# Optimization experiments

Measured on AMD Instinct MI355X. Metric: run time of the kernel, lower is better.

Reference implementation:

```python
import jax, jax.numpy as jnp
import numpy as np

NUM_HEAD = 8


def setup_inputs() -> dict:
    key = jax.random.key(0)
    k1, k2, k3, k4 = jax.random.split(key, 4)
    B, C, H, W = 16, 512, 64, 64
    x = jax.random.normal(k1, (B, C, H, W), dtype=jnp.float32)
    w_qkv = jax.random.normal(k2, (3 * C, C), dtype=jnp.float32) * 0.02  # Conv2d 1x1, no bias
    w_proj = jax.random.normal(k3, (C, C), dtype=jnp.float32) * 0.02
    b_proj = jax.random.normal(k4, (C,), dtype=jnp.float32) * 0.02
    return {"x": x, "w_qkv": w_qkv, "w_proj": w_proj, "b_proj": b_proj}


def reference(x, w_qkv, w_proj, b_proj):
    B, C, H, W = x.shape
    nh = NUM_HEAD
    hd = C // nh
    scale = hd ** (-0.5)
    # 1x1 conv == channel matmul
    qkv = jnp.einsum('oc,bchw->bohw', w_qkv, x)  # [B, 3C, H, W]
    q, k, v = jnp.split(qkv, 3, axis=1)
    q = q.reshape(B, nh, hd, H * W)
    k = k.reshape(B, nh, hd, H * W)
    v = v.reshape(B, nh, hd, H * W)
    # NOTE: faithful to source: contracts over the spatial (last) axis,
    # producing a [B, nh, hd, hd] matrix.
    attn = jnp.einsum('bnqd,bnkd->bnqk', q, k) * scale
    attn = jax.nn.softmax(attn, axis=-1)
    # Faithful to source: 'k' and 'v' are both summed independently (outer sum),
    # exactly as torch.einsum computes it.
    out = jnp.einsum('bnqk,bnvd->bnqd', attn, v)
    out = out.reshape(B, C, H, W)
    return jnp.einsum('oc,bchw->bohw', w_proj, out) + b_proj[None, :, None, None]
```

## Files before the change

### kernel.cpp

```cpp
#include <hip/hip_runtime.h>

#define CDIM 512
#define NH 8
#define HWDIM 4096
#define BATCH 16

__global__ __launch_bounds__(256) void prep_kernel(
    const float* __restrict__ wqkv, const float* __restrict__ wproj,
    float* __restrict__ wvT, float* __restrict__ wp) {
  int idx = blockIdx.x * 256 + threadIdx.x;
  if (idx < 4096) {
    int n = idx >> 9, c = idx & 511;
    const float* p = wqkv + (size_t)(1024 + n * 64) * CDIM + c;
    float s = 0.f;
#pragma unroll 8
    for (int j = 0; j < 64; ++j) s += p[(size_t)j * CDIM];
    wvT[c * 8 + n] = s;
  } else if (idx < 8192) {
    int i2 = idx - 4096;
    int n = i2 >> 9, o = i2 & 511;
    const float* p = wproj + (size_t)o * CDIM + n * 64;
    float s = 0.f;
#pragma unroll 4
    for (int j = 0; j < 16; ++j) {
      float4 v = *(const float4*)(p + j * 4);
      s += v.x + v.y + v.z + v.w;
    }
    wp[o * 8 + n] = s;
  }
}

__global__ __launch_bounds__(256) void s_kernel(
    const float* __restrict__ x, const float* __restrict__ wvT,
    float* __restrict__ S) {
  __shared__ __align__(16) float sPart[4][NH][64];

  const int t = threadIdx.x;
  const int wave = t >> 6;
  const int lane = t & 63;
  const int f = lane & 15;
  const int sub = lane >> 4;
  const int cg = wave * 4 + sub;

  const int pos0 = blockIdx.x * 64;
  const int b = pos0 >> 12;
  const int hw0 = pos0 & (HWDIM - 1);

  const float* xb = x + ((size_t)b * CDIM + (size_t)cg * 32) * HWDIM + hw0 + f * 4;
  const float* wb = wvT + cg * 32 * 8;

  float acc[NH][4];
#pragma unroll
  for (int n = 0; n < NH; ++n)
    acc[n][0] = acc[n][1] = acc[n][2] = acc[n][3] = 0.f;

#pragma unroll 8
  for (int cc = 0; cc < 32; ++cc) {
    const float4 xv = *(const float4*)(xb + (size_t)cc * HWDIM);
    const float4 w0 = *(const float4*)(wb + cc * 8);
    const float4 w1 = *(const float4*)(wb + cc * 8 + 4);
    const float wn[8] = {w0.x, w0.y, w0.z, w0.w, w1.x, w1.y, w1.z, w1.w};
    const float xv4[4] = {xv.x, xv.y, xv.z, xv.w};
#pragma unroll
    for (int n = 0; n < NH; ++n)
#pragma unroll
      for (int p = 0; p < 4; ++p) acc[n][p] = fmaf(wn[n], xv4[p], acc[n][p]);
  }

#pragma unroll
  for (int n = 0; n < NH; ++n)
#pragma unroll
    for (int p = 0; p < 4; ++p) {
      float v = acc[n][p];
      v += __shfl_xor(v, 16, 64);
      v += __shfl_xor(v, 32, 64);
      acc[n][p] = v;
    }

  if (sub == 0) {
#pragma unroll
    for (int n = 0; n < NH; ++n)
      *(float4*)&sPart[wave][n][f * 4] =
          make_float4(acc[n][0], acc[n][1], acc[n][2], acc[n][3]);
  }
  __syncthreads();

#pragma unroll
  for (int r = 0; r < 2; ++r) {
    const int v = t + r * 256;
    const int n = v >> 6, sp = v & 63;
    const float s =
        sPart[0][n][sp] + sPart[1][n][sp] + sPart[2][n][sp] + sPart[3][n][sp];
    S[(size_t)b * NH * HWDIM + (size_t)n * HWDIM + hw0 + sp] = s;
  }
}

__global__ __launch_bounds__(256) void y_kernel(
    const float* __restrict__ S, const float* __restrict__ wp,
    const float* __restrict__ bias, float* __restrict__ y) {
  const int t = threadIdx.x;
  const int wave = t >> 6;
  const int lane = t & 63;
  const int f = lane & 15;
  const int og = wave * 4 + (lane >> 4);

  const int pos0 = blockIdx.x * 64;
  const int b = pos0 >> 12;
  const int hw0 = pos0 & (HWDIM - 1);

  float4 Sv[NH];
#pragma unroll
  for (int n = 0; n < NH; ++n)
    Sv[n] = *(const float4*)(S + (size_t)b * NH * HWDIM + (size_t)n * HWDIM + hw0 + f * 4);

  float* yb = y + ((size_t)b * CDIM + (size_t)og * 32) * HWDIM + hw0 + f * 4;
  const float* wb = wp + og * 32 * 8;
  const float* bb = bias + og * 32;

#pragma unroll 4
  for (int i = 0; i < 32; ++i) {
    const float4 w0 = *(const float4*)(wb + i * 8);
    const float4 w1 = *(const float4*)(wb + i * 8 + 4);
    const float wn[8] = {w0.x, w0.y, w0.z, w0.w, w1.x, w1.y, w1.z, w1.w};
    const float b0 = bb[i];
    float r[4] = {b0, b0, b0, b0};
#pragma unroll
    for (int n = 0; n < NH; ++n) {
      r[0] = fmaf(wn[n], Sv[n].x, r[0]);
      r[1] = fmaf(wn[n], Sv[n].y, r[1]);
      r[2] = fmaf(wn[n], Sv[n].z, r[2]);
      r[3] = fmaf(wn[n], Sv[n].w, r[3]);
    }
    *(float4*)(yb + (size_t)i * HWDIM) = make_float4(r[0], r[1], r[2], r[3]);
  }
}

extern "C" void kernel_launch(void* const* d_in, const int* in_sizes, int n_in,
                              void* d_out, int out_size, void* d_ws, size_t ws_size,
                              hipStream_t stream) {
  const float* x     = (const float*)d_in[0];
  const float* wqkv  = (const float*)d_in[1];
  const float* wproj = (const float*)d_in[2];
  const float* bproj = (const float*)d_in[3];
  float* y = (float*)d_out;

  float* wvT = (float*)d_ws;
  float* wp  = wvT + 4096;
  float* S   = wp + 4096;

  prep_kernel<<<32, 256, 0, stream>>>(wqkv, wproj, wvT, wp);
  s_kernel<<<1024, 256, 0, stream>>>(x, wvT, S);
  y_kernel<<<1024, 256, 0, stream>>>(S, wp, bproj, y);
}
```

Baseline: 281.0 us.

## Split channel reduction across blocks with partial sums and widen spatial tiles

The S reduction over channels is split into four channel groups, each handled by its own block. Each block covers 256 spatial positions with full 64-lane float4 coverage and writes a partial result to a separate slice of workspace. The y kernel now reads and sums the four partials before the projection, and each y block covers 128 output channels over 256 positions. This removes the cross-lane shuffle reduction and gives wider contiguous rows. The cost is four times the intermediate S traffic plus an extra reduction step in y_kernel.

```diff
diff --git a/kernel.cpp b/kernel.cpp
--- a/kernel.cpp
+++ b/kernel.cpp
@@ -4,6 +4,8 @@
 #define NH 8
 #define HWDIM 4096
 #define BATCH 16
+#define PTILE 256
+#define PSTRIDE (BATCH * NH * HWDIM)
 
 __global__ __launch_bounds__(256) void prep_kernel(
     const float* __restrict__ wqkv, const float* __restrict__ wproj,
@@ -30,24 +32,23 @@
   }
 }
 
-__global__ __launch_bounds__(256) void s_kernel(
+__global__ __launch_bounds__(256, 4) void s_part_kernel(
     const float* __restrict__ x, const float* __restrict__ wvT,
-    float* __restrict__ S) {
-  __shared__ __align__(16) float sPart[4][NH][64];
+    float* __restrict__ pS) {
+  __shared__ __align__(16) float sPart[4][NH][PTILE];
 
   const int t = threadIdx.x;
   const int wave = t >> 6;
   const int lane = t & 63;
-  const int f = lane & 15;
-  const int sub = lane >> 4;
-  const int cg = wave * 4 + sub;
+  const int bx = blockIdx.x;
+  const int pt = bx & 255;
+  const int cg = bx >> 8;
+  const int b = pt >> 4;
+  const int hw0 = (pt & 15) << 8;
 
-  const int pos0 = blockIdx.x * 64;
-  const int b = pos0 >> 12;
-  const int hw0 = pos0 & (HWDIM - 1);
-
-  const float* xb = x + ((size_t)b * CDIM + (size_t)cg * 32) * HWDIM + hw0 + f * 4;
-  const float* wb = wvT + cg * 32 * 8;
+  const int c0 = cg * 128 + wave * 32;
+  const float* xb = x + ((size_t)b * CDIM + c0) * HWDIM + hw0 + lane * 4;
+  const float* wb = wvT + c0 * 8;
 
   float acc[NH][4];
 #pragma unroll
@@ -69,53 +70,49 @@
 
 #pragma unroll
   for (int n = 0; n < NH; ++n)
-#pragma unroll
-    for (int p = 0; p < 4; ++p) {
-      float v = acc[n][p];
-      v += __shfl_xor(v, 16, 64);
-      v += __shfl_xor(v, 32, 64);
-      acc[n][p] = v;
-    }
-
-  if (sub == 0) {
-#pragma unroll
-    for (int n = 0; n < NH; ++n)
-      *(float4*)&sPart[wave][n][f * 4] =
-          make_float4(acc[n][0], acc[n][1], acc[n][2], acc[n][3]);
-  }
+    *(float4*)&sPart[wave][n][lane * 4] =
+        make_float4(acc[n][0], acc[n][1], acc[n][2], acc[n][3]);
   __syncthreads();
 
+  float* out = pS + (size_t)cg * PSTRIDE + ((size_t)b * NH) * HWDIM + hw0;
 #pragma unroll
-  for (int r = 0; r < 2; ++r) {
-    const int v = t + r * 256;
-    const int n = v >> 6, sp = v & 63;
-    const float s =
+  for (int r = 0; r < 8; ++r) {
+    const int i = t + r * 256;
+    const int n = i >> 8, sp = i & 255;
+    const float v =
         sPart[0][n][sp] + sPart[1][n][sp] + sPart[2][n][sp] + sPart[3][n][sp];
-    S[(size_t)b * NH * HWDIM + (size_t)n * HWDIM + hw0 + sp] = s;
+    out[(size_t)n * HWDIM + sp] = v;
   }
 }
 
-__global__ __launch_bounds__(256) void y_kernel(
-    const float* __restrict__ S, const float* __restrict__ wp,
+__global__ __launch_bounds__(256, 4) void y_kernel(
+    const float* __restrict__ pS, const float* __restrict__ wp,
     const float* __restrict__ bias, float* __restrict__ y) {
   const int t = threadIdx.x;
   const int wave = t >> 6;
   const int lane = t & 63;
-  const int f = lane & 15;
-  const int og = wave * 4 + (lane >> 4);
-
-  const int pos0 = blockIdx.x * 64;
-  const int b = pos0 >> 12;
-  const int hw0 = pos0 & (HWDIM - 1);
+  const int bx = blockIdx.x;
+  const int pt = bx & 255;
+  const int og = bx >> 8;
+  const int b = pt >> 4;
+  const int hw0 = (pt & 15) << 8;
 
   float4 Sv[NH];
 #pragma unroll
-  for (int n = 0; n < NH; ++n)
-    Sv[n] = *(const float4*)(S + (size_t)b * NH * HWDIM + (size_t)n * HWDIM + hw0 + f * 4);
+  for (int n = 0; n < NH; ++n) {
+    const float* p = pS + ((size_t)b * NH + n) * HWDIM + hw0 + lane * 4;
+    const float4 a0 = *(const float4*)(p);
+    const float4 a1 = *(const float4*)(p + PSTRIDE);
+    const float4 a2 = *(const float4*)(p + 2 * (size_t)PSTRIDE);
+    const float4 a3 = *(const float4*)(p + 3 * (size_t)PSTRIDE);
+    Sv[n] = make_float4(a0.x + a1.x + a2.x + a3.x, a0.y + a1.y + a2.y + a3.y,
+                        a0.z + a1.z + a2.z + a3.z, a0.w + a1.w + a2.w + a3.w);
+  }
 
-  float* yb = y + ((size_t)b * CDIM + (size_t)og * 32) * HWDIM + hw0 + f * 4;
-  const float* wb = wp + og * 32 * 8;
-  const float* bb = bias + og * 32;
+  const int o0 = og * 128 + wave * 32;
+  const float* wb = wp + o0 * 8;
+  const float* bb = bias + o0;
+  float* yb = y + ((size_t)b * CDIM + o0) * HWDIM + hw0 + lane * 4;
 
 #pragma unroll 4
   for (int i = 0; i < 32; ++i) {
@@ -146,9 +143,9 @@
 
   float* wvT = (float*)d_ws;
   float* wp  = wvT + 4096;
-  float* S   = wp + 4096;
+  float* pS  = wp + 4096;
 
   prep_kernel<<<32, 256, 0, stream>>>(wqkv, wproj, wvT, wp);
-  s_kernel<<<1024, 256, 0, stream>>>(x, wvT, S);
-  y_kernel<<<1024, 256, 0, stream>>>(S, wp, bproj, y);
+  s_part_kernel<<<1024, 256, 0, stream>>>(x, wvT, pS);
+  y_kernel<<<1024, 256, 0, stream>>>(pS, wp, bproj, y);
 }
```

Measured after the change: 280.8 us. Within noise of the previous version (-0.0%).
